# Kernel optimization log

Measured on AMD Instinct MI355X. Metric: run time of the kernel, lower is better.

## Reference

```python
import jax, jax.numpy as jnp
import numpy as np

B, N, D_IN, D_OUT = 4, 512, 128, 64
TEMP = 1.0
BN_EPS = 1e-5


def setup_inputs() -> dict:
    key = jax.random.key(0)
    ks = jax.random.split(key, 9)
    return {
        "x": jax.random.normal(ks[0], (B, N, D_IN), jnp.float32),
        "att_proj_w": jax.random.normal(ks[1], (D_OUT, D_IN), jnp.float32) * 0.08,
        "att_proj_b": jax.random.normal(ks[2], (D_OUT,), jnp.float32) * 0.01,
        "att_weight": jax.random.normal(ks[3], (D_OUT, 1), jnp.float32) * 0.15,
        "proj_with_att_w": jax.random.normal(ks[4], (D_OUT, D_IN), jnp.float32) * 0.08,
        "proj_with_att_b": jax.random.normal(ks[5], (D_OUT,), jnp.float32) * 0.01,
        "proj_without_att_w": jax.random.normal(ks[6], (D_OUT, D_IN), jnp.float32) * 0.08,
        "proj_without_att_b": jax.random.normal(ks[7], (D_OUT,), jnp.float32) * 0.01,
        "bn_gamma": jnp.ones((D_OUT,), jnp.float32),
        "bn_beta": jnp.zeros((D_OUT,), jnp.float32),
    }


def reference(x, att_proj_w, att_proj_b, att_weight,
              proj_with_att_w, proj_with_att_b,
              proj_without_att_w, proj_without_att_b,
              bn_gamma, bn_beta):
    # Dropout is identity (inference). Pairwise node multiplication: (B,N,N,D_in)
    pair = x[:, :, None, :] * x[:, None, :, :]
    # Linear + tanh on the pairwise tensor -> (B,N,N,D_out)
    a = jnp.tanh(jnp.einsum('bijd,od->bijo', pair, att_proj_w) + att_proj_b)
    # Score via learned vector, temperature, softmax over second node axis (torch dim=-2 of (B,N,N,1))
    scores = jnp.einsum('bijo,o->bij', a, att_weight[:, 0]) / TEMP
    att = jax.nn.softmax(scores, axis=2)  # normalize over j
    # Attention-weighted aggregation + two projections (torch Linear: x @ W.T + b)
    agg = jnp.einsum('bij,bjd->bid', att, x)
    h = (agg @ proj_with_att_w.T + proj_with_att_b) \
        + (x @ proj_without_att_w.T + proj_without_att_b)
    # BatchNorm1d (training-mode batch stats) over flattened (B*N, D_out)
    hf = h.reshape(-1, h.shape[-1])
    mean = hf.mean(axis=0)
    var = hf.var(axis=0)  # biased, as torch BN uses for normalization
    y = (hf - mean) / jnp.sqrt(var + BN_EPS) * bn_gamma + bn_beta
    y = y.reshape(h.shape)
    return jax.nn.selu(y)
```

## Files before the change

### kernel.cpp

```cpp
#include <hip/hip_runtime.h>
#include <math.h>

#define NB 4
#define NN 512
#define DIN 128
#define DOUT 64
#define TI 2
#define CHROWS 64
#define NCHL 4
#define NTOT (NB * NN)

typedef __attribute__((ext_vector_type(8))) short short8;
typedef __attribute__((ext_vector_type(8))) unsigned short ushort8;
typedef __attribute__((ext_vector_type(16))) float f32x16;

__device__ __forceinline__ unsigned short f2bf(float f) {
    union { float f; unsigned u; } v; v.f = f;
    unsigned r = v.u + 0x7fffu + ((v.u >> 16) & 1u);
    return (unsigned short)(r >> 16);
}

__device__ __forceinline__ float bf2f(unsigned short u) {
    union { unsigned u; float f; } v; v.u = ((unsigned)u) << 16; return v.f;
}

__global__ void x_to_bf16(const float* __restrict__ x, unsigned short* __restrict__ xbf) {
    const int idx = blockIdx.x * 256 + threadIdx.x;
    float4 v = ((const float4*)x)[idx];
    ushort4 o;
    o.x = f2bf(v.x); o.y = f2bf(v.y); o.z = f2bf(v.z); o.w = f2bf(v.w);
    ((ushort4*)xbf)[idx] = o;
}

__global__ __launch_bounds__(256, 3) void gat_main(
    const float* __restrict__ x,
    const unsigned short* __restrict__ xbf,
    const float* __restrict__ apw,
    const float* __restrict__ apb,
    const float* __restrict__ attw,
    float* __restrict__ pnum,
    float* __restrict__ pden)
{
    __shared__ unsigned short xt[2][CHROWS * DIN];
    __shared__ float scp[2][TI][256];
    __shared__ float xis[TI][DIN];
    __shared__ float red_s[4][TI];

    float* pagg = (float*)&xt[0][0];

    const int t = threadIdx.x;
    const int blk = blockIdx.x;
    const int jh = blk & 1;
    const int rp = blk >> 1;
    const int b = rp >> 8;
    const int rowbase = (rp & 255) * TI;
    const int rid0 = rp * TI;
    const float* xb = x + (size_t)b * NN * DIN;
    const unsigned short* xbb = xbf + (size_t)b * NN * DIN;

    {
        const int i = t >> 7, d = t & 127;
        xis[i][d] = xb[(size_t)(rowbase + i) * DIN + d];
    }

    const int lane = t & 63, wid = t >> 6;
    const int qi = wid & 1;
    const int oh = wid >> 1;
    const int l31 = lane & 31;
    const int hi = lane >> 5;

    const int r0 = t >> 4, g0 = t & 15;
    const int st_off0 = r0 * 256 + ((g0 ^ (r0 & 7)) << 4);

    int rdoff[8];
    #pragma unroll
    for (int ks = 0; ks < 8; ++ks)
        rdoff[ks] = l31 * 256 + (((ks * 2 + hi) ^ (l31 & 7)) << 4);

    const ushort8* gsrc = (const ushort8*)xbb + (size_t)jh * 4096;
    ushort8 nv0 = gsrc[t];
    ushort8 nv1 = gsrc[256 + t];
    ushort8 nv2 = gsrc[512 + t];
    ushort8 nv3 = gsrc[768 + t];
    __syncthreads();

    short8 afr[8];
    {
        const float* wrow = apw + (size_t)(oh * 32 + l31) * DIN;
        const float* xk0 = &xis[qi][0];
        #pragma unroll
        for (int ks = 0; ks < 8; ++ks) {
            const int k0 = ks * 16 + hi * 8;
            float4 w0 = *(const float4*)(wrow + k0);
            float4 w1 = *(const float4*)(wrow + k0 + 4);
            const float* xk = xk0 + k0;
            short8 fr;
            fr[0] = (short)f2bf(w0.x * xk[0]);
            fr[1] = (short)f2bf(w0.y * xk[1]);
            fr[2] = (short)f2bf(w0.z * xk[2]);
            fr[3] = (short)f2bf(w0.w * xk[3]);
            fr[4] = (short)f2bf(w1.x * xk[4]);
            fr[5] = (short)f2bf(w1.y * xk[5]);
            fr[6] = (short)f2bf(w1.z * xk[6]);
            fr[7] = (short)f2bf(w1.w * xk[7]);
            afr[ks] = fr;
        }
    }

    const float C2 = 2.885390081777927f;
    float awm2[16], abc[16], sumw = 0.0f;
    #pragma unroll
    for (int r = 0; r < 16; ++r) {
        const int crow = (r & 3) + 8 * (r >> 2) + 4 * hi;
        const int o = oh * 32 + crow;
        float wv = attw[o], bv = apb[o];
        awm2[r] = -2.0f * wv;
        abc[r] = bv * C2;
        sumw += wv;
    }

#define WRITES(BUF) do {                                                        \
    *(ushort8*)((char*)&xt[BUF][0] + st_off0) = nv0;                            \
    *(ushort8*)((char*)&xt[BUF][0] + st_off0 + 4096) = nv1;                     \
    *(ushort8*)((char*)&xt[BUF][0] + st_off0 + 8192) = nv2;                     \
    *(ushort8*)((char*)&xt[BUF][0] + st_off0 + 12288) = nv3;                    \
} while (0)

#define LOADR(CH) do {                                                          \
    nv0 = gsrc[(CH) * 1024 + t];                                                \
    nv1 = gsrc[(CH) * 1024 + 256 + t];                                          \
    nv2 = gsrc[(CH) * 1024 + 512 + t];                                          \
    nv3 = gsrc[(CH) * 1024 + 768 + t];                                          \
} while (0)

#define COMPUTE(ACC, BUF, S) do {                                               \
    f32x16 zz_ = {0.f,0.f,0.f,0.f,0.f,0.f,0.f,0.f,                              \
                  0.f,0.f,0.f,0.f,0.f,0.f,0.f,0.f};                             \
    ACC = zz_;                                                                  \
    _Pragma("unroll")                                                           \
    for (int ks_ = 0; ks_ < 8; ++ks_) {                                         \
        short8 bk_ = *(const short8*)((const char*)&xt[BUF][0] +                \
                                      rdoff[ks_] + (S) * 8192);                 \
        ACC = __builtin_amdgcn_mfma_f32_32x32x16_bf16(afr[ks_], bk_, ACC, 0, 0, 0); \
    }                                                                           \
} while (0)

#define POST(ACC, I32) do {                                                     \
    float sp_ = sumw;                                                           \
    _Pragma("unroll")                                                           \
    for (int r_ = 0; r_ < 16; ++r_) {                                           \
        float arg_ = fmaf(ACC[r_], C2, abc[r_]);                                \
        float u_, rc_;                                                          \
        asm("v_exp_f32 %0, %1" : "=v"(u_) : "v"(arg_));                         \
        float den_ = u_ + 1.0f;                                                 \
        asm("v_rcp_f32 %0, %1" : "=v"(rc_) : "v"(den_));                        \
        sp_ = fmaf(awm2[r_], rc_, sp_);                                         \
    }                                                                           \
    sp_ += __shfl_xor(sp_, 32);                                                 \
    if (lane < 32) scp[oh][qi][(I32) * 32 + l31] = sp_;                         \
} while (0)

    f32x16 a0, a1;

    WRITES(0);
    __syncthreads();

    LOADR(1);
    COMPUTE(a0, 0, 0);
    COMPUTE(a1, 0, 1);
    POST(a0, 0);
    POST(a1, 1);
    WRITES(1);
    __syncthreads();
    LOADR(2);
    COMPUTE(a0, 1, 0);
    COMPUTE(a1, 1, 1);
    POST(a0, 2);
    POST(a1, 3);
    WRITES(0);
    __syncthreads();
    LOADR(3);
    COMPUTE(a0, 0, 0);
    COMPUTE(a1, 0, 1);
    POST(a0, 4);
    POST(a1, 5);
    WRITES(1);
    __syncthreads();
    COMPUTE(a0, 1, 0);
    COMPUTE(a1, 1, 1);
    POST(a0, 6);
    POST(a1, 7);
    __syncthreads();

    {
        float s0 = scp[0][0][t] + scp[1][0][t];
        float s1 = scp[0][1][t] + scp[1][1][t];
        float e0 = __expf(s0), e1 = __expf(s1);
        scp[0][0][t] = e0;
        scp[0][1][t] = e1;
        float ss0 = e0, ss1 = e1;
        #pragma unroll
        for (int m = 1; m < 64; m <<= 1) {
            ss0 += __shfl_xor(ss0, m);
            ss1 += __shfl_xor(ss1, m);
        }
        if (lane == 0) { red_s[wid][0] = ss0; red_s[wid][1] = ss1; }
    }
    __syncthreads();
    if (t < TI) {
        float den = red_s[0][t] + red_s[1][t] + red_s[2][t] + red_s[3][t];
        pden[jh * NTOT + rid0 + t] = den;
    }

    const float* esc0 = &scp[0][0][0];
    const float* esc1 = &scp[0][1][0];
    {
        const int d0 = (t & 31) * 4, q = t >> 5;
        const unsigned short* xc = xbb + (size_t)(jh * 256) * DIN + d0;
        float b0[4] = {0.f, 0.f, 0.f, 0.f};
        float b1[4] = {0.f, 0.f, 0.f, 0.f};
        #pragma unroll 4
        for (int jj = q * 32; jj < q * 32 + 32; ++jj) {
            ushort4 xv = *(const ushort4*)(xc + (size_t)jj * DIN);
            float e0v = esc0[jj], e1v = esc1[jj];
            float x0 = bf2f(xv.x), x1 = bf2f(xv.y);
            float x2 = bf2f(xv.z), x3 = bf2f(xv.w);
            b0[0] = fmaf(e0v, x0, b0[0]); b0[1] = fmaf(e0v, x1, b0[1]);
            b0[2] = fmaf(e0v, x2, b0[2]); b0[3] = fmaf(e0v, x3, b0[3]);
            b1[0] = fmaf(e1v, x0, b1[0]); b1[1] = fmaf(e1v, x1, b1[1]);
            b1[2] = fmaf(e1v, x2, b1[2]); b1[3] = fmaf(e1v, x3, b1[3]);
        }
        #pragma unroll
        for (int c = 0; c < 4; ++c) {
            pagg[(q * TI + 0) * DIN + d0 + c] = b0[c];
            pagg[(q * TI + 1) * DIN + d0 + c] = b1[c];
        }
    }
    __syncthreads();
    {
        const int i = t >> 7, d = t & 127;
        float s = 0.f;
        #pragma unroll
        for (int q = 0; q < 8; ++q) s += pagg[(q * TI + i) * DIN + d];
        pnum[(size_t)(jh * NTOT + rid0 + i) * DIN + d] = s;
    }
#undef COMPUTE
#undef POST
#undef LOADR
#undef WRITES
}

__global__ __launch_bounds__(256, 2) void combine_proj(
    const float* __restrict__ x,
    const float* __restrict__ pnum, const float* __restrict__ pden,
    const float* __restrict__ pww, const float* __restrict__ pwb,
    const float* __restrict__ pow_, const float* __restrict__ pob,
    float* __restrict__ out, float* __restrict__ pbn)
{
    __shared__ float wL[DOUT][DIN + 1];
    __shared__ float vL[16][DIN];
    __shared__ float invL[16];
    __shared__ float psum[4][DOUT];
    __shared__ float psum2[4][DOUT];

    const int t = threadIdx.x;
    const int rbase = blockIdx.x * 16;
    const int o = t & 63, rq = t >> 6;

    for (int k = t; k < DOUT * DIN; k += 256) wL[k >> 7][k & 127] = pww[k];
    for (int k = t; k < 16 * DIN; k += 256) {
        const int i = k >> 7, d = k & 127;
        const int r = rbase + i;
        vL[i][d] = pnum[(size_t)r * DIN + d] + pnum[(size_t)(NTOT + r) * DIN + d];
    }
    if (t < 16) {
        const int r = rbase + t;
        invL[t] = 1.0f / (pden[r] + pden[NTOT + r]);
    }
    __syncthreads();

    float accp[4] = {0.f, 0.f, 0.f, 0.f};
    #pragma unroll 4
    for (int d = 0; d < DIN; ++d) {
        float w = wL[o][d];
        #pragma unroll
        for (int rr = 0; rr < 4; ++rr)
            accp[rr] = fmaf(w, vL[rq + rr * 4][d], accp[rr]);
    }
    __syncthreads();

    for (int k = t; k < DOUT * DIN; k += 256) wL[k >> 7][k & 127] = pow_[k];
    for (int k = t; k < 16 * DIN; k += 256) {
        const int i = k >> 7, d = k & 127;
        vL[i][d] = x[(size_t)(rbase + i) * DIN + d];
    }
    __syncthreads();

    float res[4] = {0.f, 0.f, 0.f, 0.f};
    #pragma unroll 4
    for (int d = 0; d < DIN; ++d) {
        float w = wL[o][d];
        #pragma unroll
        for (int rr = 0; rr < 4; ++rr)
            res[rr] = fmaf(w, vL[rq + rr * 4][d], res[rr]);
    }
    const float bias = pwb[o] + pob[o];
    float ls = 0.f, ls2 = 0.f;
    #pragma unroll
    for (int rr = 0; rr < 4; ++rr) {
        const int i = rq + rr * 4;
        float h = accp[rr] * invL[i] + res[rr] + bias;
        out[(size_t)(rbase + i) * DOUT + o] = h;
        ls += h; ls2 += h * h;
    }
    psum[rq][o] = ls;
    psum2[rq][o] = ls2;
    __syncthreads();
    if (t < DOUT) {
        pbn[((size_t)blockIdx.x * 2 + 0) * DOUT + t] =
            psum[0][t] + psum[1][t] + psum[2][t] + psum[3][t];
        pbn[((size_t)blockIdx.x * 2 + 1) * DOUT + t] =
            psum2[0][t] + psum2[1][t] + psum2[2][t] + psum2[3][t];
    }
}

__global__ void bn_finish(const float* __restrict__ pbn, float* __restrict__ stats) {
    __shared__ float ps[4][DOUT], ps2[4][DOUT];
    const int t = threadIdx.x;
    const int c = t & 63, grp = t >> 6;
    float s = 0.f, s2 = 0.f;
    for (int bb = grp * 32; bb < grp * 32 + 32; ++bb) {
        s += pbn[((size_t)bb * 2 + 0) * DOUT + c];
        s2 += pbn[((size_t)bb * 2 + 1) * DOUT + c];
    }
    ps[grp][c] = s;
    ps2[grp][c] = s2;
    __syncthreads();
    if (t < DOUT) {
        const float inv_n = 1.0f / (float)NTOT;
        float ss = ps[0][t] + ps[1][t] + ps[2][t] + ps[3][t];
        float ss2 = ps2[0][t] + ps2[1][t] + ps2[2][t] + ps2[3][t];
        float mean = ss * inv_n;
        float var = ss2 * inv_n - mean * mean;
        stats[t] = mean;
        stats[DOUT + t] = rsqrtf(var + 1e-5f);
    }
}

__global__ void bn_selu(float* __restrict__ out, const float* __restrict__ stats,
                        const float* __restrict__ gamma, const float* __restrict__ beta) {
    const int idx = blockIdx.x * 256 + threadIdx.x;
    const int c = idx & 63;
    float v = out[idx];
    float y = (v - stats[c]) * stats[DOUT + c] * gamma[c] + beta[c];
    const float scale = 1.0507009873554805f;
    const float alpha = 1.6732632423543772f;
    out[idx] = y > 0.0f ? scale * y : scale * alpha * (__expf(y) - 1.0f);
}

extern "C" void kernel_launch(void* const* d_in, const int* in_sizes, int n_in,
                              void* d_out, int out_size, void* d_ws, size_t ws_size,
                              hipStream_t stream) {
    const float* x    = (const float*)d_in[0];
    const float* apw  = (const float*)d_in[1];
    const float* apb  = (const float*)d_in[2];
    const float* attw = (const float*)d_in[3];
    const float* pww  = (const float*)d_in[4];
    const float* pwb  = (const float*)d_in[5];
    const float* pow_ = (const float*)d_in[6];
    const float* pob  = (const float*)d_in[7];
    const float* gmm  = (const float*)d_in[8];
    const float* bta  = (const float*)d_in[9];
    float* out = (float*)d_out;

    char* ws = (char*)d_ws;
    float* stats = (float*)ws;
    unsigned short* xbf = (unsigned short*)(ws + 1024);
    float* pnum = (float*)(ws + 528384);
    float* pden = (float*)(ws + 528384 + 2097152);
    float* pbn  = (float*)(ws + 528384 + 2097152 + 16384);

    x_to_bf16<<<256, 256, 0, stream>>>(x, xbf);
    gat_main<<<2 * NTOT / TI, 256, 0, stream>>>(x, xbf, apw, apb, attw, pnum, pden);
    combine_proj<<<NTOT / 16, 256, 0, stream>>>(x, pnum, pden, pww, pwb, pow_, pob,
                                                out, pbn);
    bn_finish<<<1, 256, 0, stream>>>(pbn, stats);
    bn_selu<<<(NTOT * DOUT) / 256, 256, 0, stream>>>(out, stats, gmm, bta);
}
```

Before: 69.01 us.

## Stage x tiles via direct global-to-LDS loads and fuse BN finish into SELU

Result: faster. 64.83 us (-6.1%).

```diff
diff --git a/kernel.cpp b/kernel.cpp
--- a/kernel.cpp
+++ b/kernel.cpp
@@ -13,6 +13,9 @@
 typedef __attribute__((ext_vector_type(8))) short short8;
 typedef __attribute__((ext_vector_type(8))) unsigned short ushort8;
 typedef __attribute__((ext_vector_type(16))) float f32x16;
+
+typedef __attribute__((address_space(3))) unsigned int lds_u32;
+typedef __attribute__((address_space(1))) unsigned int glb_u32;
 
 __device__ __forceinline__ unsigned short f2bf(float f) {
     union { float f; unsigned u; } v; v.f = f;
@@ -57,11 +60,7 @@
     const int rid0 = rp * TI;
     const float* xb = x + (size_t)b * NN * DIN;
     const unsigned short* xbb = xbf + (size_t)b * NN * DIN;
-
-    {
-        const int i = t >> 7, d = t & 127;
-        xis[i][d] = xb[(size_t)(rowbase + i) * DIN + d];
-    }
+    const char* gsrcb = (const char*)xbb + (size_t)jh * 65536;
 
     const int lane = t & 63, wid = t >> 6;
     const int qi = wid & 1;
@@ -69,20 +68,27 @@
     const int l31 = lane & 31;
     const int hi = lane >> 5;
 
-    const int r0 = t >> 4, g0 = t & 15;
-    const int st_off0 = r0 * 256 + ((g0 ^ (r0 & 7)) << 4);
+#define STAGE(BUF, CH) do {                                                     \
+    _Pragma("unroll")                                                           \
+    for (int k_ = 0; k_ < 4; ++k_) {                                            \
+        const char* ga_ = gsrcb + (CH) * 16384 +                                \
+            (k_ * 16 + (t >> 4)) * 256 + (((t & 15) ^ ((t >> 4) & 7)) << 4);    \
+        lds_u32* lp_ = (lds_u32*)((char*)&xt[BUF][0] + k_ * 4096 + wid * 1024); \
+        __builtin_amdgcn_global_load_lds((const glb_u32*)ga_, lp_, 16, 0, 0);   \
+    }                                                                           \
+} while (0)
+
+    {
+        const int i = t >> 7, d = t & 127;
+        xis[i][d] = xb[(size_t)(rowbase + i) * DIN + d];
+    }
+    STAGE(0, 0);
+    __syncthreads();
 
     int rdoff[8];
     #pragma unroll
     for (int ks = 0; ks < 8; ++ks)
         rdoff[ks] = l31 * 256 + (((ks * 2 + hi) ^ (l31 & 7)) << 4);
-
-    const ushort8* gsrc = (const ushort8*)xbb + (size_t)jh * 4096;
-    ushort8 nv0 = gsrc[t];
-    ushort8 nv1 = gsrc[256 + t];
-    ushort8 nv2 = gsrc[512 + t];
-    ushort8 nv3 = gsrc[768 + t];
-    __syncthreads();
 
     short8 afr[8];
     {
@@ -119,20 +125,6 @@
         sumw += wv;
     }
 
-#define WRITES(BUF) do {                                                        \
-    *(ushort8*)((char*)&xt[BUF][0] + st_off0) = nv0;                            \
-    *(ushort8*)((char*)&xt[BUF][0] + st_off0 + 4096) = nv1;                     \
-    *(ushort8*)((char*)&xt[BUF][0] + st_off0 + 8192) = nv2;                     \
-    *(ushort8*)((char*)&xt[BUF][0] + st_off0 + 12288) = nv3;                    \
-} while (0)
-
-#define LOADR(CH) do {                                                          \
-    nv0 = gsrc[(CH) * 1024 + t];                                                \
-    nv1 = gsrc[(CH) * 1024 + 256 + t];                                          \
-    nv2 = gsrc[(CH) * 1024 + 512 + t];                                          \
-    nv3 = gsrc[(CH) * 1024 + 768 + t];                                          \
-} while (0)
-
 #define COMPUTE(ACC, BUF, S) do {                                               \
     f32x16 zz_ = {0.f,0.f,0.f,0.f,0.f,0.f,0.f,0.f,                              \
                   0.f,0.f,0.f,0.f,0.f,0.f,0.f,0.f};                             \
@@ -162,29 +154,23 @@
 
     f32x16 a0, a1;
 
-    WRITES(0);
-    __syncthreads();
-
-    LOADR(1);
+    STAGE(1, 1);
     COMPUTE(a0, 0, 0);
     COMPUTE(a1, 0, 1);
     POST(a0, 0);
     POST(a1, 1);
-    WRITES(1);
-    __syncthreads();
-    LOADR(2);
+    __syncthreads();
+    STAGE(0, 2);
     COMPUTE(a0, 1, 0);
     COMPUTE(a1, 1, 1);
     POST(a0, 2);
     POST(a1, 3);
-    WRITES(0);
-    __syncthreads();
-    LOADR(3);
+    __syncthreads();
+    STAGE(1, 3);
     COMPUTE(a0, 0, 0);
     COMPUTE(a1, 0, 1);
     POST(a0, 4);
     POST(a1, 5);
-    WRITES(1);
     __syncthreads();
     COMPUTE(a0, 1, 0);
     COMPUTE(a1, 1, 1);
@@ -246,8 +232,7 @@
     }
 #undef COMPUTE
 #undef POST
-#undef LOADR
-#undef WRITES
+#undef STAGE
 }
 
 __global__ __launch_bounds__(256, 2) void combine_proj(
@@ -324,17 +309,22 @@
     }
 }
 
-__global__ void bn_finish(const float* __restrict__ pbn, float* __restrict__ stats) {
+__global__ __launch_bounds__(256) void bn_selu(
+    float* __restrict__ out, const float* __restrict__ pbn,
+    const float* __restrict__ gamma, const float* __restrict__ beta) {
     __shared__ float ps[4][DOUT], ps2[4][DOUT];
+    __shared__ float stats[2][DOUT];
     const int t = threadIdx.x;
-    const int c = t & 63, grp = t >> 6;
-    float s = 0.f, s2 = 0.f;
-    for (int bb = grp * 32; bb < grp * 32 + 32; ++bb) {
-        s += pbn[((size_t)bb * 2 + 0) * DOUT + c];
-        s2 += pbn[((size_t)bb * 2 + 1) * DOUT + c];
-    }
-    ps[grp][c] = s;
-    ps2[grp][c] = s2;
+    {
+        const int c = t & 63, grp = t >> 6;
+        float s = 0.f, s2 = 0.f;
+        for (int bb = grp * 32; bb < grp * 32 + 32; ++bb) {
+            s += pbn[((size_t)bb * 2 + 0) * DOUT + c];
+            s2 += pbn[((size_t)bb * 2 + 1) * DOUT + c];
+        }
+        ps[grp][c] = s;
+        ps2[grp][c] = s2;
+    }
     __syncthreads();
     if (t < DOUT) {
         const float inv_n = 1.0f / (float)NTOT;
@@ -342,17 +332,14 @@
         float ss2 = ps2[0][t] + ps2[1][t] + ps2[2][t] + ps2[3][t];
         float mean = ss * inv_n;
         float var = ss2 * inv_n - mean * mean;
-        stats[t] = mean;
-        stats[DOUT + t] = rsqrtf(var + 1e-5f);
-    }
-}
-
-__global__ void bn_selu(float* __restrict__ out, const float* __restrict__ stats,
-                        const float* __restrict__ gamma, const float* __restrict__ beta) {
-    const int idx = blockIdx.x * 256 + threadIdx.x;
+        stats[0][t] = mean;
+        stats[1][t] = rsqrtf(var + 1e-5f);
+    }
+    __syncthreads();
+    const int idx = blockIdx.x * 256 + t;
     const int c = idx & 63;
     float v = out[idx];
-    float y = (v - stats[c]) * stats[DOUT + c] * gamma[c] + beta[c];
+    float y = (v - stats[0][c]) * stats[1][c] * gamma[c] + beta[c];
     const float scale = 1.0507009873554805f;
     const float alpha = 1.6732632423543772f;
     out[idx] = y > 0.0f ? scale * y : scale * alpha * (__expf(y) - 1.0f);
@@ -374,7 +361,6 @@
     float* out = (float*)d_out;
 
     char* ws = (char*)d_ws;
-    float* stats = (float*)ws;
     unsigned short* xbf = (unsigned short*)(ws + 1024);
     float* pnum = (float*)(ws + 528384);
     float* pden = (float*)(ws + 528384 + 2097152);
@@ -384,6 +370,5 @@
     gat_main<<<2 * NTOT / TI, 256, 0, stream>>>(x, xbf, apw, apb, attw, pnum, pden);
     combine_proj<<<NTOT / 16, 256, 0, stream>>>(x, pnum, pden, pww, pwb, pow_, pob,
                                                 out, pbn);
-    bn_finish<<<1, 256, 0, stream>>>(pbn, stats);
-    bn_selu<<<(NTOT * DOUT) / 256, 256, 0, stream>>>(out, stats, gmm, bta);
-}
+    bn_selu<<<(NTOT * DOUT) / 256, 256, 0, stream>>>(out, pbn, gmm, bta);
+}
```
